# Kernel tuning notes

Hardware: AMD Instinct MI355X
Metric: run time of the kernel (lower is better)

Reference implementation:

```python
import jax, jax.numpy as jnp
import numpy as np
from jax import lax

L, C, H, W = 3, 64, 32, 32   # layer_num, new_size channels/spatial
N = H * W                    # 1024 attention positions
B = 8


def _conv(x, w, b, stride, pad):
    out = lax.conv_general_dilated(
        x, w, (stride, stride), [(pad, pad), (pad, pad)],
        dimension_numbers=('NCHW', 'OIHW', 'NCHW'))
    return out + b[None, :, None, None]


def setup_inputs() -> dict:
    key = jax.random.key(0)
    ks = iter(jax.random.split(key, 40))
    def rn(shape, scale=1.0):
        return (jax.random.normal(next(ks), shape) * scale).astype(jnp.float32)
    inp = {
        'src0': rn((B, 128, 64, 64)), 'src1': rn((B, 256, 32, 32)), 'src2': rn((B, 512, 32, 32)),
        'tgt0': rn((B, 128, 64, 64)), 'tgt1': rn((B, 256, 32, 32)), 'tgt2': rn((B, 512, 32, 32)),
    }
    # Project/Fit convs: layer0 is stride-2 3x3 (64->32), layers 1,2 are 1x1
    for pre, ic, k in [('fs0', 128, 3), ('fs1', 256, 1), ('fs2', 512, 1),
                       ('ft0', 128, 3), ('ft1', 256, 1), ('ft2', 512, 1)]:
        inp[pre + '_w'] = rn((C, ic, k, k), (ic * k * k) ** -0.5)
        inp[pre + '_b'] = rn((C,), 0.01)
    # PAM query/key/value and CAM value 1x1 convs, stacked over layers
    for pre in ['pq', 'pk', 'pv', 'cv']:
        inp[pre + '_w'] = rn((L, C, C), C ** -0.5)
        inp[pre + '_b'] = rn((L, C), 0.01)
    return inp


def reference(src0, src1, src2, tgt0, tgt1, tgt2,
              fs0_w, fs0_b, fs1_w, fs1_b, fs2_w, fs2_b,
              ft0_w, ft0_b, ft1_w, ft1_b, ft2_w, ft2_b,
              pq_w, pq_b, pk_w, pk_b, pv_w, pv_b, cv_w, cv_b):
    # Project: Fit each source/target to [B,C,H,W]
    S = jnp.stack([_conv(src0, fs0_w, fs0_b, 2, 1),
                   _conv(src1, fs1_w, fs1_b, 1, 0),
                   _conv(src2, fs2_w, fs2_b, 1, 0)])   # [L,B,C,H,W]
    T = jnp.stack([_conv(tgt0, ft0_w, ft0_b, 2, 1),
                   _conv(tgt1, ft1_w, ft1_b, 1, 0),
                   _conv(tgt2, ft2_w, ft2_b, 1, 0)])
    S = S.reshape(L, B, C, N)
    T = T.reshape(L, B, C, N)

    # ---- PAM: position attention over all (target i, source j) pairs ----
    q = jnp.einsum('ioc,ibcn->ibon', pq_w, T) + pq_b[:, None, :, None]
    k = jnp.einsum('joc,jbcn->jbon', pk_w, S) + pk_b[:, None, :, None]
    v = jnp.einsum('ioc,ibcn->ibon', pv_w, T) + pv_b[:, None, :, None]
    e_pam = jnp.einsum('ibcn,jbcm->ijbnm', q, k)          # [L,L,B,N,N]
    alpha_pam = jax.nn.softmax(lax.stop_gradient(e_pam.mean(axis=(2, 3, 4))), axis=-1)
    attn_pam = jax.nn.softmax(e_pam, axis=-1).sum(axis=1)  # sum over sources j -> [L,B,N,N]
    # out[b,c,n] = sum_m v[b,c,m] * attn[b,n,m]  (value @ attention^T)
    out_pam = jnp.einsum('ibcm,ibnm->ibcn', v, attn_pam)

    # ---- CAM: channel attention over all pairs ----
    e_cam = jnp.einsum('ibcn,jbdn->ijbcd', T, S)           # [L,L,B,C,C]
    alpha_cam = jax.nn.softmax(lax.stop_gradient(e_cam.mean(axis=(2, 3, 4))), axis=-1)
    attn_cam = jax.nn.softmax(e_cam, axis=-1).sum(axis=1)  # [L,B,C,C]
    vc = jnp.einsum('ioc,ibcn->ibon', cv_w, T) + cv_b[:, None, :, None]
    out_cam = jnp.einsum('ibcd,ibdn->ibcn', attn_cam, vc)

    fused = ((out_pam + out_cam) * 0.5).reshape(L, B, C * N)
    alpha = (alpha_cam + alpha_pam) * 0.5                  # [L,L]
    srcs = S.reshape(L, B, C * N)
    # DAAttention appends fused_i then projected target_i per layer (order preserved)
    tgts = jnp.stack([fused, T.reshape(L, B, C * N)], axis=1).reshape(2 * L, B, C * N)
    return (srcs, alpha, tgts)
```

## Files before the change

kernel.cpp:

```cpp
#include <hip/hip_runtime.h>

static constexpr int L_ = 3, B_ = 8, C_ = 64, N_ = 1024;
static constexpr int PLANE = C_ * N_;
static constexpr int SZ    = L_ * B_ * PLANE;
static constexpr int BPL   = B_ * PLANE;

#define DI __device__ __forceinline__

typedef _Float16 h8 __attribute__((ext_vector_type(8)));
typedef __attribute__((ext_vector_type(4))) float f32x4;
typedef unsigned int uint32;

DI float wred_sum(float v) {
#pragma unroll
  for (int m = 1; m < 64; m <<= 1) v += __shfl_xor(v, m, 64);
  return v;
}

DI unsigned short f2h(float f) {
  return __builtin_bit_cast(unsigned short, (_Float16)f);
}
DI uint32 pkh(float a, float b) {
  return (uint32)f2h(a) | ((uint32)f2h(b) << 16);
}
DI h8 bch8(uint4 v) { return __builtin_bit_cast(h8, v); }

DI f32x4 mfmah(h8 a, h8 b, f32x4 c) {
  return __builtin_amdgcn_mfma_f32_16x16x32_f16(a, b, c, 0, 0, 0);
}

__global__ __launch_bounds__(256) void xprep_kernel(
    const float* __restrict__ in, unsigned short* __restrict__ out, int K, int N)
{
  const int g = blockIdx.x, kc = blockIdx.y, nc = blockIdx.z;
  const int t = threadIdx.x;
  __shared__ float tl[64][65];
  const float* ing = in + (size_t)g * K * N + (size_t)(kc * 64) * N + nc * 64;
#pragma unroll 4
  for (int r = 0; r < 16; ++r) {
    const int kk = r * 4 + (t >> 6);
    tl[kk][t & 63] = ing[(size_t)kk * N + (t & 63)];
  }
  __syncthreads();
  const int mm = t >> 2, kseg = (t & 3) * 16;
  uint32 hw[8];
#pragma unroll
  for (int ii = 0; ii < 8; ++ii)
    hw[ii] = pkh(tl[kseg + 2 * ii][mm], tl[kseg + 2 * ii + 1][mm]);
  unsigned short* o = out + ((size_t)g * N + nc * 64 + mm) * K + kc * 64 + kseg;
  uint4 h0; h0.x = hw[0]; h0.y = hw[1]; h0.z = hw[2]; h0.w = hw[3];
  uint4 h1; h1.x = hw[4]; h1.y = hw[5]; h1.z = hw[6]; h1.w = hw[7];
  *reinterpret_cast<uint4*>(o)     = h0;
  *reinterpret_cast<uint4*>(o + 8) = h1;
}

__global__ __launch_bounds__(256) void w9conv_kernel(
    const float* __restrict__ w_s, const float* __restrict__ w_t,
    unsigned short* __restrict__ w9_s, unsigned short* __restrict__ w9_t)
{
  const int e = blockIdx.x * 256 + threadIdx.x;
  const float* w = (e < 73728) ? w_s : w_t;
  unsigned short* o = (e < 73728) ? w9_s : w9_t;
  const int le = (e < 73728) ? e : e - 73728;
  const int ci = le & 127;
  const int q = le >> 7;
  const int co = q & 63;
  const int k9 = q >> 6;
  o[le] = f2h(w[(co * 128 + ci) * 9 + k9]);
}

__global__ __launch_bounds__(256) void conv0_mfma_kernel(
    const unsigned short* __restrict__ inT_s, const unsigned short* __restrict__ inT_t,
    const unsigned short* __restrict__ w9_s, const unsigned short* __restrict__ w9_t,
    const float* __restrict__ b_s, const float* __restrict__ b_t,
    float* __restrict__ Sout, float* __restrict__ Tout, float* __restrict__ tdup)
{
  const int yr = blockIdx.x;
  const int b  = blockIdx.y;
  const int st = blockIdx.z;
  const unsigned short* inT = st ? inT_t : inT_s;
  const unsigned short* w9  = st ? w9_t  : w9_s;
  const float* bias = st ? b_t : b_s;
  float* outA = st ? Tout : Sout;

  const int t = threadIdx.x, lane = t & 63;
  const int ct = t >> 6;
  const int nl = lane & 15, g16 = lane >> 4;
  const unsigned short* inb = inT + (size_t)b * (4096 * 128);
  const unsigned short* wbase = w9 + (size_t)(ct * 16 + nl) * 128;

  f32x4 acc0 = f32x4{0.f, 0.f, 0.f, 0.f};
  f32x4 acc1 = f32x4{0.f, 0.f, 0.f, 0.f};
  const uint4 zz = uint4{0u, 0u, 0u, 0u};

#pragma unroll 1
  for (int tap = 0; tap < 9; ++tap) {
    const int ky = tap / 3, kx = tap - 3 * (tap / 3);
    const int py = 2 * yr - 1 + ky;
    const int px0 = 2 * nl - 1 + kx;
    const int px1 = px0 + 32;
    const bool v0 = (py >= 0) && (px0 >= 0);
    const bool v1 = (py >= 0);
    const unsigned short* prow = inb + (ptrdiff_t)py * (64 * 128);
#pragma unroll
    for (int ks = 0; ks < 4; ++ks) {
      const h8 a = bch8(*reinterpret_cast<const uint4*>(
          wbase + tap * 8192 + ks * 32 + g16 * 8));
      const uint4 bv0 = v0 ? *reinterpret_cast<const uint4*>(
                                 prow + px0 * 128 + ks * 32 + g16 * 8) : zz;
      const uint4 bv1 = v1 ? *reinterpret_cast<const uint4*>(
                                 prow + px1 * 128 + ks * 32 + g16 * 8) : zz;
      acc0 = mfmah(a, bch8(bv0), acc0);
      acc1 = mfmah(a, bch8(bv1), acc1);
    }
  }

  const int yb = yr * 32;
#pragma unroll
  for (int r = 0; r < 4; ++r) {
    const int co = ct * 16 + g16 * 4 + r;
    const float bv = bias[co];
    const int idx = (b * 64 + co) * 1024 + yb + nl;
    const float o0 = acc0[r] + bv;
    const float o1 = acc1[r] + bv;
    outA[idx] = o0; outA[idx + 16] = o1;
    if (st) { tdup[idx] = o0; tdup[idx + 16] = o1; }
  }
}

__global__ __launch_bounds__(256) void gemm64_kernel(
    const float* __restrict__ W, int wstride, int wdiv,
    const float* __restrict__ X, int xstride,
    float* __restrict__ out, int ostride,
    const float* __restrict__ bias, int bstride,
    int K)
{
  const int g  = blockIdx.x;
  const int n0 = blockIdx.y * 64;
  const float* Wg = W + (size_t)(g / wdiv) * wstride;
  const float* Xg = X + (size_t)g * xstride;
  const int t = threadIdx.x;
  __shared__ float Xs[32][64];
  __shared__ float Ws[32][64];
  const int tn = t & 15, cgp = t >> 4;
  const int n4 = tn * 4, co4 = cgp * 4;
  float acc[4][4] = {};

  for (int k0 = 0; k0 < K; k0 += 32) {
    {
      const int kk = t >> 4;
      const int nn = (t & 15) * 4;
      *reinterpret_cast<float4*>(&Xs[kk][nn]) =
          *reinterpret_cast<const float4*>(Xg + (size_t)(k0 + kk) * N_ + n0 + nn);
      *reinterpret_cast<float4*>(&Xs[kk + 16][nn]) =
          *reinterpret_cast<const float4*>(Xg + (size_t)(k0 + kk + 16) * N_ + n0 + nn);
    }
    {
      const int co = t & 63, q4 = t >> 6;
      const float* wp = Wg + (size_t)co * K + k0 + q4 * 8;
      const float4 a = *reinterpret_cast<const float4*>(wp);
      const float4 c = *reinterpret_cast<const float4*>(wp + 4);
      const int kb = q4 * 8;
      Ws[kb + 0][co] = a.x; Ws[kb + 1][co] = a.y; Ws[kb + 2][co] = a.z; Ws[kb + 3][co] = a.w;
      Ws[kb + 4][co] = c.x; Ws[kb + 5][co] = c.y; Ws[kb + 6][co] = c.z; Ws[kb + 7][co] = c.w;
    }
    __syncthreads();
#pragma unroll
    for (int kk = 0; kk < 32; ++kk) {
      const float4 xv = *reinterpret_cast<const float4*>(&Xs[kk][n4]);
      const float4 wv = *reinterpret_cast<const float4*>(&Ws[kk][co4]);
      const float xa[4] = {xv.x, xv.y, xv.z, xv.w};
      const float wa[4] = {wv.x, wv.y, wv.z, wv.w};
#pragma unroll
      for (int a = 0; a < 4; ++a)
#pragma unroll
        for (int b2 = 0; b2 < 4; ++b2)
          acc[a][b2] = fmaf(wa[a], xa[b2], acc[a][b2]);
    }
    __syncthreads();
  }

  float bv[4] = {0.f, 0.f, 0.f, 0.f};
  if (bias) {
    const float* bg = bias + (size_t)(g / wdiv) * bstride;
    bv[0] = bg[co4]; bv[1] = bg[co4 + 1]; bv[2] = bg[co4 + 2]; bv[3] = bg[co4 + 3];
  }
#pragma unroll
  for (int ii = 0; ii < 4; ++ii) {
    float4 o4;
    o4.x = acc[ii][0] + bv[ii]; o4.y = acc[ii][1] + bv[ii];
    o4.z = acc[ii][2] + bv[ii]; o4.w = acc[ii][3] + bv[ii];
    *reinterpret_cast<float4*>(out + (size_t)g * ostride + (co4 + ii) * N_ + n0 + n4) = o4;
  }
}

__global__ __launch_bounds__(256) void proj_kernel(
    const float* __restrict__ Tm, const float* __restrict__ Sm,
    const float* __restrict__ wq, const float* __restrict__ wk,
    const float* __restrict__ wv2, const float* __restrict__ wc,
    const float* __restrict__ bq, const float* __restrict__ bk,
    const float* __restrict__ bv2, const float* __restrict__ bc,
    float* __restrict__ outbase)
{
  const int g  = blockIdx.x;
  const int n0 = blockIdx.y * 64;
  const int z  = blockIdx.z;
  const float* W  = (z == 0) ? wq : (z == 1) ? wk : (z == 2) ? wv2 : wc;
  const float* bi = (z == 0) ? bq : (z == 1) ? bk : (z == 2) ? bv2 : bc;
  const float* Xg = ((z == 1) ? Sm : Tm) + (size_t)g * PLANE;
  float* out = outbase + (size_t)z * SZ + (size_t)g * PLANE;
  const float* Wg = W + (g >> 3) * 4096;
  const float* bg = bi + (g >> 3) * 64;

  const int t = threadIdx.x;
  __shared__ float Xs[32][64];
  __shared__ float Ws[32][64];
  const int tn = t & 15, cgp = t >> 4;
  const int n4 = tn * 4, co4 = cgp * 4;
  float acc[4][4] = {};

#pragma unroll 1
  for (int k0 = 0; k0 < 64; k0 += 32) {
    {
      const int kk = t >> 4;
      const int nn = (t & 15) * 4;
      *reinterpret_cast<float4*>(&Xs[kk][nn]) =
          *reinterpret_cast<const float4*>(Xg + (size_t)(k0 + kk) * N_ + n0 + nn);
      *reinterpret_cast<float4*>(&Xs[kk + 16][nn]) =
          *reinterpret_cast<const float4*>(Xg + (size_t)(k0 + kk + 16) * N_ + n0 + nn);
    }
    {
      const int co = t & 63, q4 = t >> 6;
      const float* wp = Wg + (size_t)co * 64 + k0 + q4 * 8;
      const float4 a = *reinterpret_cast<const float4*>(wp);
      const float4 c = *reinterpret_cast<const float4*>(wp + 4);
      const int kb = q4 * 8;
      Ws[kb + 0][co] = a.x; Ws[kb + 1][co] = a.y; Ws[kb + 2][co] = a.z; Ws[kb + 3][co] = a.w;
      Ws[kb + 4][co] = c.x; Ws[kb + 5][co] = c.y; Ws[kb + 6][co] = c.z; Ws[kb + 7][co] = c.w;
    }
    __syncthreads();
#pragma unroll
    for (int kk = 0; kk < 32; ++kk) {
      const float4 xv = *reinterpret_cast<const float4*>(&Xs[kk][n4]);
      const float4 wv = *reinterpret_cast<const float4*>(&Ws[kk][co4]);
      const float xa[4] = {xv.x, xv.y, xv.z, xv.w};
      const float wa[4] = {wv.x, wv.y, wv.z, wv.w};
#pragma unroll
      for (int a = 0; a < 4; ++a)
#pragma unroll
        for (int b2 = 0; b2 < 4; ++b2)
          acc[a][b2] = fmaf(wa[a], xa[b2], acc[a][b2]);
    }
    __syncthreads();
  }

#pragma unroll
  for (int ii = 0; ii < 4; ++ii) {
    const float bv = bg[co4 + ii];
    float4 o4;
    o4.x = acc[ii][0] + bv; o4.y = acc[ii][1] + bv;
    o4.z = acc[ii][2] + bv; o4.w = acc[ii][3] + bv;
    *reinterpret_cast<float4*>(out + (co4 + ii) * N_ + n0 + n4) = o4;
  }
}

__global__ __launch_bounds__(256) void whconv_kernel(
    const float* __restrict__ w1s, const float* __restrict__ w2s,
    const float* __restrict__ w1t, const float* __restrict__ w2t,
    unsigned short* __restrict__ wh)
{
  const int p = blockIdx.x * 256 + threadIdx.x;
  const float* in; int local; unsigned short* out;
  if (p < 8192)       { in = w1s; local = p;         out = wh; }
  else if (p < 24576) { in = w2s; local = p - 8192;  out = wh + 16384; }
  else if (p < 32768) { in = w1t; local = p - 24576; out = wh + 49152; }
  else                { in = w2t; local = p - 32768; out = wh + 65536; }
  const float2 v = *reinterpret_cast<const float2*>(in + 2 * local);
  *reinterpret_cast<uint32*>(out + 2 * local) = pkh(v.x, v.y);
}

__global__ __launch_bounds__(256) void gemmh_kernel(
    const unsigned short* __restrict__ Xa, const unsigned short* __restrict__ Xb,
    const unsigned short* __restrict__ Wa, const unsigned short* __restrict__ Wb,
    const float* __restrict__ ba, const float* __restrict__ bb,
    float* __restrict__ oa, float* __restrict__ ob, float* __restrict__ o2b,
    int K)
{
  const int g = blockIdx.x;
  const bool isb = g >= 8;
  const int gl = g & 7;
  const unsigned short* X = (isb ? Xb : Xa) + (size_t)gl * 1024 * K;
  const unsigned short* W = isb ? Wb : Wa;
  const float* bias = isb ? bb : ba;
  float* out = (isb ? ob : oa) + (size_t)gl * PLANE;
  float* out2 = isb ? o2b + (size_t)gl * PLANE : nullptr;

  const int t = threadIdx.x, lane = t & 63, wv = t >> 6;
  const int nl = lane & 15, g16 = lane >> 4;
  const int n0w = blockIdx.y * 64 + wv * 16;

  const unsigned short* xp = X + (size_t)(n0w + nl) * K + g16 * 8;
  const unsigned short* wp = W + (size_t)nl * K + g16 * 8;

  f32x4 acc[4];
#pragma unroll
  for (int ct = 0; ct < 4; ++ct) acc[ct] = f32x4{0.f, 0.f, 0.f, 0.f};

#pragma unroll 4
  for (int kk = 0; kk < K; kk += 32) {
    const h8 a = bch8(*reinterpret_cast<const uint4*>(xp + kk));
#pragma unroll
    for (int ct = 0; ct < 4; ++ct) {
      const h8 bfr = bch8(*reinterpret_cast<const uint4*>(wp + (size_t)ct * 16 * K + kk));
      acc[ct] = mfmah(a, bfr, acc[ct]);
    }
  }

#pragma unroll
  for (int ct = 0; ct < 4; ++ct) {
    const int co = ct * 16 + nl;
    const float bv = bias[co];
    float4 o4;
    o4.x = acc[ct][0] + bv; o4.y = acc[ct][1] + bv;
    o4.z = acc[ct][2] + bv; o4.w = acc[ct][3] + bv;
    const int idx = co * N_ + n0w + g16 * 4;
    *reinterpret_cast<float4*>(out + idx) = o4;
    if (out2) {
      out2[idx] = o4.x; out2[idx + 1] = o4.y;
      out2[idx + 2] = o4.z; out2[idx + 3] = o4.w;
    }
  }
}

__global__ __launch_bounds__(256) void kprep_kernel(
    const float* __restrict__ kb, const float* __restrict__ vb,
    unsigned short* __restrict__ kT, unsigned short* __restrict__ vh)
{
  const int g = blockIdx.x;
  const int ch = blockIdx.y;
  const int t = threadIdx.x;
  const float* kg = kb + (size_t)g * PLANE;
  __shared__ float tl[64][65];

#pragma unroll 1
  for (int tile = 0; tile < 4; ++tile) {
    const int m0 = ch * 256 + tile * 64;
    __syncthreads();
#pragma unroll 4
    for (int r = 0; r < 16; ++r) {
      const int c = r * 4 + (t >> 6);
      tl[c][t & 63] = kg[c * N_ + m0 + (t & 63)];
    }
    __syncthreads();
    const int mm = t >> 2, cseg = (t & 3) * 16;
    uint32 hw[8];
#pragma unroll
    for (int ii = 0; ii < 8; ++ii)
      hw[ii] = pkh(tl[cseg + 2 * ii][mm], tl[cseg + 2 * ii + 1][mm]);
    const size_t o = ((size_t)g * 1024 + m0 + mm) * 64 + cseg;
    uint4 h0; h0.x = hw[0]; h0.y = hw[1]; h0.z = hw[2]; h0.w = hw[3];
    uint4 h1; h1.x = hw[4]; h1.y = hw[5]; h1.z = hw[6]; h1.w = hw[7];
    *reinterpret_cast<uint4*>(kT + o)     = h0;
    *reinterpret_cast<uint4*>(kT + o + 8) = h1;
  }

  const float* vg = vb + (size_t)g * PLANE;
  unsigned short* vo = vh + (size_t)g * PLANE;
  for (int e8 = ch * 2048 + t; e8 < (ch + 1) * 2048; e8 += 256) {
    const float4 a = *reinterpret_cast<const float4*>(vg + (size_t)e8 * 8);
    const float4 b = *reinterpret_cast<const float4*>(vg + (size_t)e8 * 8 + 4);
    uint4 u;
    u.x = pkh(a.x, a.y); u.y = pkh(a.z, a.w);
    u.z = pkh(b.x, b.y); u.w = pkh(b.z, b.w);
    *reinterpret_cast<uint4*>(vo + (size_t)e8 * 8) = u;
  }
}

__global__ __launch_bounds__(256) void ecam_kernel(
    const float* __restrict__ T, const float* __restrict__ S,
    float* __restrict__ ecam, float* __restrict__ esum_cam)
{
  const int bx = blockIdx.x;
  const int b = bx & 7;
  const int j = (bx >> 3) % 3;
  const int i = bx / 24;
  const float* Tg = T + (size_t)(i * 8 + b) * PLANE;
  const float* Sg = S + (size_t)(j * 8 + b) * PLANE;
  const int t = threadIdx.x;
  __shared__ float Ts[64 * 68];
  __shared__ float Ss[64 * 68];
  __shared__ float rs[4];
  float acc[4][4] = {};
  const int c0 = (t & 15) * 4, d0 = (t >> 4) * 4;

  for (int nb = 0; nb < 1024; nb += 64) {
    __syncthreads();
    {
      const int nn = t & 63, rb = t >> 6;
#pragma unroll
      for (int r = 0; r < 16; ++r) {
        const int row = rb * 16 + r;
        Ts[nn * 68 + row] = Tg[row * N_ + nb + nn];
        Ss[nn * 68 + row] = Sg[row * N_ + nb + nn];
      }
    }
    __syncthreads();
#pragma unroll 8
    for (int nn = 0; nn < 64; ++nn) {
      const float4 tv = *reinterpret_cast<const float4*>(&Ts[nn * 68 + c0]);
      const float4 sv = *reinterpret_cast<const float4*>(&Ss[nn * 68 + d0]);
      const float ta[4] = {tv.x, tv.y, tv.z, tv.w};
      const float sa[4] = {sv.x, sv.y, sv.z, sv.w};
#pragma unroll
      for (int ci = 0; ci < 4; ++ci)
#pragma unroll
        for (int di = 0; di < 4; ++di)
          acc[ci][di] = fmaf(ta[ci], sa[di], acc[ci][di]);
    }
  }
  float s = 0.f;
#pragma unroll
  for (int ci = 0; ci < 4; ++ci)
#pragma unroll
    for (int di = 0; di < 4; ++di) s += acc[ci][di];
  s = wred_sum(s);
  if ((t & 63) == 0) rs[t >> 6] = s;
  __syncthreads();
  if (t == 0) atomicAdd(esum_cam + i * 3 + j, rs[0] + rs[1] + rs[2] + rs[3]);

  float* eo = ecam + (size_t)((i * 3 + j) * 8 + b) * 4096;
#pragma unroll
  for (int ci = 0; ci < 4; ++ci) {
    float4 o4; o4.x = acc[ci][0]; o4.y = acc[ci][1]; o4.z = acc[ci][2]; o4.w = acc[ci][3];
    *reinterpret_cast<float4*>(eo + (c0 + ci) * 64 + d0) = o4;
  }
}

__global__ __launch_bounds__(256) void acam_kernel(
    const float* __restrict__ ecam, float* __restrict__ acam)
{
  const int bx = blockIdx.x;
  const int b = bx & 7, i = bx >> 3;
  const int t = threadIdx.x;
  const int c = t >> 2, seg = t & 3;
  float acc[16] = {};
#pragma unroll
  for (int j = 0; j < 3; ++j) {
    const float* e = ecam + (size_t)((i * 3 + j) * 8 + b) * 4096 + c * 64 + seg * 16;
    float ev[16];
#pragma unroll
    for (int r = 0; r < 4; ++r) {
      const float4 v4 = *reinterpret_cast<const float4*>(e + r * 4);
      ev[4 * r] = v4.x; ev[4 * r + 1] = v4.y; ev[4 * r + 2] = v4.z; ev[4 * r + 3] = v4.w;
    }
    float mx = ev[0];
#pragma unroll
    for (int r = 1; r < 16; ++r) mx = fmaxf(mx, ev[r]);
    mx = fmaxf(mx, __shfl_xor(mx, 1, 4));
    mx = fmaxf(mx, __shfl_xor(mx, 2, 4));
    float pv[16], ss = 0.f;
#pragma unroll
    for (int r = 0; r < 16; ++r) { pv[r] = __expf(ev[r] - mx); ss += pv[r]; }
    ss += __shfl_xor(ss, 1, 4);
    ss += __shfl_xor(ss, 2, 4);
    const float rc = 1.f / ss;
#pragma unroll
    for (int r = 0; r < 16; ++r) acc[r] += pv[r] * rc;
  }
  float* ao = acam + (size_t)(i * 8 + b) * 4096 + c * 64 + seg * 16;
#pragma unroll
  for (int r = 0; r < 4; ++r) {
    float4 o4; o4.x = acc[4 * r]; o4.y = acc[4 * r + 1]; o4.z = acc[4 * r + 2]; o4.w = acc[4 * r + 3];
    *reinterpret_cast<float4*>(ao + r * 4) = o4;
  }
}

__global__ __launch_bounds__(512, 4) void pam_mfma_kernel(
    const float* __restrict__ q, const unsigned short* __restrict__ kT,
    const unsigned short* __restrict__ vh,
    const float* __restrict__ ocam, float* __restrict__ tgts, float* __restrict__ esum_pam)
{
  const int bx = blockIdx.x;
  const int qt = bx & 63;
  const int b  = (bx >> 6) & 7;
  const int i  = bx >> 9;
  const int n0 = qt * 16;
  const int t = threadIdx.x;
  const int lane = t & 63;
  const int wv = t >> 6;
  const int nl = lane & 15;
  const int g16 = lane >> 4;

  __shared__ unsigned short Plds[16 * 1024];
  __shared__ float qlds[64 * 17];
  __shared__ float redmx[128];
  __shared__ float redse[128];
  __shared__ float redes[8];
  float* osum = qlds;

  const size_t ibo = (size_t)(i * 8 + b) * PLANE;

  const float* qg = q + ibo;
  for (int e = t; e < 1024; e += 512)
    qlds[(e >> 4) * 17 + (e & 15)] = qg[(e >> 4) * N_ + n0 + (e & 15)];
  __syncthreads();

  h8 qh[2];
#pragma unroll
  for (int ks = 0; ks < 2; ++ks) {
#pragma unroll
    for (int idx = 0; idx < 8; ++idx)
      qh[ks][idx] = (_Float16)qlds[(ks * 32 + g16 * 8 + idx) * 17 + nl];
  }

  const int wm0 = wv * 128;
  const int ct = wv & 3;
  const int mh = wv >> 2;
  const unsigned short* vg = vh + ibo + (size_t)(ct * 16 + nl) * 1024 + mh * 512 + g16 * 8;
  f32x4 oat = f32x4{0.f, 0.f, 0.f, 0.f};

#pragma unroll 1
  for (int j = 0; j < 3; ++j) {
    const unsigned short* kp =
        kT + ((size_t)(j * 8 + b) * 1024 + wm0 + nl) * 64 + g16 * 8;

    f32x4 l4[8];
#pragma unroll
    for (int tt = 0; tt < 8; ++tt) {
      const int off = tt * 1024;
      const uint4 k0 = *reinterpret_cast<const uint4*>(kp + off);
      const uint4 k1 = *reinterpret_cast<const uint4*>(kp + off + 32);
      f32x4 a = f32x4{0.f, 0.f, 0.f, 0.f};
      a = mfmah(bch8(k0), qh[0], a);
      a = mfmah(bch8(k1), qh[1], a);
      l4[tt] = a;
    }

    float pm = -3.4e38f, es = 0.f;
#pragma unroll
    for (int tt = 0; tt < 8; ++tt) {
#pragma unroll
      for (int r = 0; r < 4; ++r) { pm = fmaxf(pm, l4[tt][r]); es += l4[tt][r]; }
    }
    pm = fmaxf(pm, __shfl_xor(pm, 16, 64));
    pm = fmaxf(pm, __shfl_xor(pm, 32, 64));
    es = wred_sum(es);
    if (lane < 16) redmx[wv * 16 + lane] = pm;
    if (lane == 0) redes[wv] = es;
    __syncthreads();
    float mx = redmx[nl];
#pragma unroll
    for (int w = 1; w < 8; ++w) mx = fmaxf(mx, redmx[w * 16 + nl]);
    if (t == 0) {
      float s = 0.f;
#pragma unroll
      for (int w = 0; w < 8; ++w) s += redes[w];
      atomicAdd(esum_pam + i * 3 + j, s);
    }

    float ps = 0.f;
#pragma unroll
    for (int tt = 0; tt < 8; ++tt) {
#pragma unroll
      for (int r = 0; r < 4; ++r) {
        l4[tt][r] = __expf(l4[tt][r] - mx);
        ps += l4[tt][r];
      }
    }
#pragma unroll
    for (int tt = 0; tt < 8; ++tt) {
      const int m = wm0 + tt * 16 + g16 * 4;
      uint2 w2;
      w2.x = pkh(l4[tt][0], l4[tt][1]);
      w2.y = pkh(l4[tt][2], l4[tt][3]);
      *reinterpret_cast<uint2*>(&Plds[nl * 1024 + (m ^ (nl * 8))]) = w2;
    }
    ps += __shfl_xor(ps, 16, 64);
    ps += __shfl_xor(ps, 32, 64);
    if (lane < 16) redse[wv * 16 + lane] = ps;
    __syncthreads();
    float den = redse[nl];
#pragma unroll
    for (int w = 1; w < 8; ++w) den += redse[w * 16 + nl];
    const float rs = 1.f / den;

    f32x4 oa = f32x4{0.f, 0.f, 0.f, 0.f};
    f32x4 ob = f32x4{0.f, 0.f, 0.f, 0.f};
#pragma unroll 4
    for (int ks = 0; ks < 16; ks += 2) {
      const int ml0 = mh * 512 + ks * 32 + g16 * 8;
      const int ml1 = ml0 + 32;
      const uint4 va0 = *reinterpret_cast<const uint4*>(vg + ks * 32);
      const uint4 pf0 = *reinterpret_cast<const uint4*>(&Plds[nl * 1024 + (ml0 ^ (nl * 8))]);
      const uint4 va1 = *reinterpret_cast<const uint4*>(vg + ks * 32 + 32);
      const uint4 pf1 = *reinterpret_cast<const uint4*>(&Plds[nl * 1024 + (ml1 ^ (nl * 8))]);
      oa = mfmah(bch8(va0), bch8(pf0), oa);
      ob = mfmah(bch8(va1), bch8(pf1), ob);
    }
#pragma unroll
    for (int r = 0; r < 4; ++r) oat[r] += rs * (oa[r] + ob[r]);
  }

  if (mh == 0) {
#pragma unroll
    for (int r = 0; r < 4; ++r)
      osum[(ct * 16 + g16 * 4 + r) * 16 + nl] = oat[r];
  }
  __syncthreads();
  if (mh == 1) {
    const float* og = ocam + ibo;
    float* outg = tgts + (size_t)(2 * i * 8 + b) * PLANE;
#pragma unroll
    for (int r = 0; r < 4; ++r) {
      const int c = ct * 16 + g16 * 4 + r;
      const int idx = c * N_ + n0 + nl;
      outg[idx] = 0.5f * (oat[r] + osum[c * 16 + nl] + og[idx]);
    }
  }
}

__global__ void alpha_kernel(const float* __restrict__ esum, float* __restrict__ alpha)
{
  const int t = threadIdx.x;
  if (t >= 9) return;
  const int i = t / 3, j = t % 3;
  float p[3], c[3];
#pragma unroll
  for (int jj = 0; jj < 3; ++jj) {
    p[jj] = esum[i * 3 + jj] * (1.0f / 8388608.0f);
    c[jj] = esum[9 + i * 3 + jj] * (1.0f / 32768.0f);
  }
  const float mp = fmaxf(p[0], fmaxf(p[1], p[2]));
  const float mc = fmaxf(c[0], fmaxf(c[1], c[2]));
  float sp = 0.f, sc = 0.f;
#pragma unroll
  for (int jj = 0; jj < 3; ++jj) { sp += __expf(p[jj] - mp); sc += __expf(c[jj] - mc); }
  alpha[t] = 0.5f * (__expf(p[j] - mp) / sp + __expf(c[j] - mc) / sc);
}

extern "C" void kernel_launch(void* const* d_in, const int* in_sizes, int n_in,
                              void* d_out, int out_size, void* d_ws, size_t ws_size,
                              hipStream_t stream)
{
  const float* src0 = (const float*)d_in[0];
  const float* src1 = (const float*)d_in[1];
  const float* src2 = (const float*)d_in[2];
  const float* tgt0 = (const float*)d_in[3];
  const float* tgt1 = (const float*)d_in[4];
  const float* tgt2 = (const float*)d_in[5];
  const float* fs0_w = (const float*)d_in[6];  const float* fs0_b = (const float*)d_in[7];
  const float* fs1_w = (const float*)d_in[8];  const float* fs1_b = (const float*)d_in[9];
  const float* fs2_w = (const float*)d_in[10]; const float* fs2_b = (const float*)d_in[11];
  const float* ft0_w = (const float*)d_in[12]; const float* ft0_b = (const float*)d_in[13];
  const float* ft1_w = (const float*)d_in[14]; const float* ft1_b = (const float*)d_in[15];
  const float* ft2_w = (const float*)d_in[16]; const float* ft2_b = (const float*)d_in[17];
  const float* pq_w = (const float*)d_in[18];  const float* pq_b = (const float*)d_in[19];
  const float* pk_w = (const float*)d_in[20];  const float* pk_b = (const float*)d_in[21];
  const float* pv_w = (const float*)d_in[22];  const float* pv_b = (const float*)d_in[23];
  const float* cv_w = (const float*)d_in[24];  const float* cv_b = (const float*)d_in[25];

  float* out = (float*)d_out;
  float* S     = out;
  float* alpha = out + SZ;
  float* tgts  = out + SZ + 9;

  float* ws   = (float*)d_ws;
  float* T    = ws;
  float* qb   = ws + (size_t)SZ;
  float* kb   = ws + (size_t)2 * SZ;
  float* vb   = ws + (size_t)3 * SZ;
  float* vcb  = ws + (size_t)4 * SZ;
  float* ocam = ws + (size_t)5 * SZ;
  float* ecam = ws + (size_t)6 * SZ;
  float* acam = ws + (size_t)6 * SZ + 294912;
  float* esum = ws + (size_t)6 * SZ + 393216;

  unsigned short* kT = (unsigned short*)(ws + (size_t)6 * SZ + 393216 + 256);
  unsigned short* vh = kT + (size_t)24 * PLANE;
  unsigned short* wh = vh + (size_t)24 * PLANE;
  unsigned short* w9s = wh + 98304;
  unsigned short* w9t = w9s + 73728;

  unsigned short* inTs = (unsigned short*)qb;
  unsigned short* inTt = inTs + 4194304;
  unsigned short* Xs1 = (unsigned short*)qb;
  unsigned short* Xs2 = Xs1 + 2097152;
  unsigned short* Xt1 = Xs1 + 6291456;
  unsigned short* Xt2 = Xs1 + 8388608;

  hipMemsetAsync(esum, 0, 18 * sizeof(float), stream);

  w9conv_kernel<<<576, 256, 0, stream>>>(fs0_w, ft0_w, w9s, w9t);
  xprep_kernel<<<dim3(8, 2, 64), 256, 0, stream>>>(src0, inTs, 128, 4096);
  xprep_kernel<<<dim3(8, 2, 64), 256, 0, stream>>>(tgt0, inTt, 128, 4096);
  conv0_mfma_kernel<<<dim3(32, 8, 2), 256, 0, stream>>>(
      inTs, inTt, w9s, w9t, fs0_b, ft0_b, S, T, tgts + (size_t)1 * BPL);

  xprep_kernel<<<dim3(8, 4, 16), 256, 0, stream>>>(src1, Xs1, 256, 1024);
  xprep_kernel<<<dim3(8, 8, 16), 256, 0, stream>>>(src2, Xs2, 512, 1024);
  xprep_kernel<<<dim3(8, 4, 16), 256, 0, stream>>>(tgt1, Xt1, 256, 1024);
  xprep_kernel<<<dim3(8, 8, 16), 256, 0, stream>>>(tgt2, Xt2, 512, 1024);
  whconv_kernel<<<192, 256, 0, stream>>>(fs1_w, fs2_w, ft1_w, ft2_w, wh);
  gemmh_kernel<<<dim3(16, 16), 256, 0, stream>>>(
      Xs1, Xt1, wh, wh + 49152, fs1_b, ft1_b,
      S + BPL, T + BPL, tgts + (size_t)3 * BPL, 256);
  gemmh_kernel<<<dim3(16, 16), 256, 0, stream>>>(
      Xs2, Xt2, wh + 16384, wh + 65536, fs2_b, ft2_b,
      S + 2 * BPL, T + 2 * BPL, tgts + (size_t)5 * BPL, 512);

  proj_kernel<<<dim3(24, 16, 4), 256, 0, stream>>>(
      T, S, pq_w, pk_w, pv_w, cv_w, pq_b, pk_b, pv_b, cv_b, qb);

  kprep_kernel<<<dim3(24, 4), 256, 0, stream>>>(kb, vb, kT, vh);

  ecam_kernel<<<72, 256, 0, stream>>>(T, S, ecam, esum + 9);
  acam_kernel<<<24, 256, 0, stream>>>(ecam, acam);
  gemm64_kernel<<<dim3(24, 16), 256, 0, stream>>>(acam, 4096, 1, vcb, PLANE, ocam, PLANE,
                                                  nullptr, 0, 64);

  pam_mfma_kernel<<<1536, 512, 0, stream>>>(qb, kT, vh, ocam, tgts, esum);

  alpha_kernel<<<1, 64, 0, stream>>>(esum, alpha);
}
```

Before: 364.5 us.

## Rewrite PAM attention as single-wave flash-style kernel with online softmax

The PAM attention kernel used 512-thread blocks where 8 waves split the key dimension and synchronized through LDS for max/sum reductions. It now runs one 64-lane wave per 16-query tile, streaming keys in chunks of 128 with an online (running-max) softmax and accumulating all 64 output channels in registers. This removes block-level barriers and the cross-wave output merge, and shrinks LDS to a small per-wave buffer. In exchange each wave does 8x more sequential work, the rescale cost is added, and there are far fewer waves in flight per CU to hide memory latency.

Result: slower. 416.1 us (+14.2%).

```diff
diff --git a/kernel.cpp b/kernel.cpp
--- a/kernel.cpp
+++ b/kernel.cpp
@@ -475,146 +475,132 @@
   }
 }
 
-__global__ __launch_bounds__(512, 4) void pam_mfma_kernel(
+__global__ __launch_bounds__(64, 2) void pam_flash_kernel(
     const float* __restrict__ q, const unsigned short* __restrict__ kT,
     const unsigned short* __restrict__ vh,
     const float* __restrict__ ocam, float* __restrict__ tgts, float* __restrict__ esum_pam)
 {
-  const int bx = blockIdx.x;
-  const int qt = bx & 63;
-  const int b  = (bx >> 6) & 7;
-  const int i  = bx >> 9;
+  const int tile = blockIdx.x;
+  const int qt = tile & 63;
+  const int b  = (tile >> 6) & 7;
+  const int i  = tile >> 9;
   const int n0 = qt * 16;
-  const int t = threadIdx.x;
-  const int lane = t & 63;
-  const int wv = t >> 6;
+  const int lane = threadIdx.x & 63;
   const int nl = lane & 15;
   const int g16 = lane >> 4;
 
-  __shared__ unsigned short Plds[16 * 1024];
-  __shared__ float qlds[64 * 17];
-  __shared__ float redmx[128];
-  __shared__ float redse[128];
-  __shared__ float redes[8];
-  float* osum = qlds;
+  __shared__ unsigned short Pw[16 * 128];
 
   const size_t ibo = (size_t)(i * 8 + b) * PLANE;
 
-  const float* qg = q + ibo;
-  for (int e = t; e < 1024; e += 512)
-    qlds[(e >> 4) * 17 + (e & 15)] = qg[(e >> 4) * N_ + n0 + (e & 15)];
-  __syncthreads();
-
+  const float* qg = q + ibo + n0 + nl;
   h8 qh[2];
 #pragma unroll
   for (int ks = 0; ks < 2; ++ks) {
 #pragma unroll
     for (int idx = 0; idx < 8; ++idx)
-      qh[ks][idx] = (_Float16)qlds[(ks * 32 + g16 * 8 + idx) * 17 + nl];
-  }
-
-  const int wm0 = wv * 128;
-  const int ct = wv & 3;
-  const int mh = wv >> 2;
-  const unsigned short* vg = vh + ibo + (size_t)(ct * 16 + nl) * 1024 + mh * 512 + g16 * 8;
-  f32x4 oat = f32x4{0.f, 0.f, 0.f, 0.f};
+      qh[ks][idx] = (_Float16)qg[(size_t)(ks * 32 + g16 * 8 + idx) * N_];
+  }
+
+  f32x4 oat[4];
+#pragma unroll
+  for (int ct = 0; ct < 4; ++ct) oat[ct] = f32x4{0.f, 0.f, 0.f, 0.f};
 
 #pragma unroll 1
   for (int j = 0; j < 3; ++j) {
-    const unsigned short* kp =
-        kT + ((size_t)(j * 8 + b) * 1024 + wm0 + nl) * 64 + g16 * 8;
-
-    f32x4 l4[8];
-#pragma unroll
-    for (int tt = 0; tt < 8; ++tt) {
-      const int off = tt * 1024;
-      const uint4 k0 = *reinterpret_cast<const uint4*>(kp + off);
-      const uint4 k1 = *reinterpret_cast<const uint4*>(kp + off + 32);
-      f32x4 a = f32x4{0.f, 0.f, 0.f, 0.f};
-      a = mfmah(bch8(k0), qh[0], a);
-      a = mfmah(bch8(k1), qh[1], a);
-      l4[tt] = a;
-    }
-
-    float pm = -3.4e38f, es = 0.f;
-#pragma unroll
-    for (int tt = 0; tt < 8; ++tt) {
-#pragma unroll
-      for (int r = 0; r < 4; ++r) { pm = fmaxf(pm, l4[tt][r]); es += l4[tt][r]; }
-    }
-    pm = fmaxf(pm, __shfl_xor(pm, 16, 64));
-    pm = fmaxf(pm, __shfl_xor(pm, 32, 64));
+    const unsigned short* kj = kT + ((size_t)(j * 8 + b) * 1024 + nl) * 64 + g16 * 8;
+    float runmx = -3.4e38f, den = 0.f, es = 0.f;
+    f32x4 oacc[4];
+#pragma unroll
+    for (int ct = 0; ct < 4; ++ct) oacc[ct] = f32x4{0.f, 0.f, 0.f, 0.f};
+
+#pragma unroll 1
+    for (int mc = 0; mc < 8; ++mc) {
+      const unsigned short* kp = kj + (size_t)(mc * 128) * 64;
+
+      f32x4 l4[8];
+#pragma unroll
+      for (int tt = 0; tt < 8; ++tt) {
+        const int off = tt * 1024;
+        const uint4 k0 = *reinterpret_cast<const uint4*>(kp + off);
+        const uint4 k1 = *reinterpret_cast<const uint4*>(kp + off + 32);
+        f32x4 a = f32x4{0.f, 0.f, 0.f, 0.f};
+        a = mfmah(bch8(k0), qh[0], a);
+        a = mfmah(bch8(k1), qh[1], a);
+        l4[tt] = a;
+      }
+
+      float cm = -3.4e38f, cs = 0.f;
+#pragma unroll
+      for (int tt = 0; tt < 8; ++tt) {
+#pragma unroll
+        for (int r = 0; r < 4; ++r) { cm = fmaxf(cm, l4[tt][r]); cs += l4[tt][r]; }
+      }
+      es += cs;
+      cm = fmaxf(cm, __shfl_xor(cm, 16, 64));
+      cm = fmaxf(cm, __shfl_xor(cm, 32, 64));
+      const float newmx = fmaxf(runmx, cm);
+      const float sc = __expf(runmx - newmx);
+
+      float psum = 0.f;
+#pragma unroll
+      for (int tt = 0; tt < 8; ++tt) {
+#pragma unroll
+        for (int r = 0; r < 4; ++r) {
+          l4[tt][r] = __expf(l4[tt][r] - newmx);
+          psum += l4[tt][r];
+        }
+      }
+      den = den * sc + psum;
+#pragma unroll
+      for (int ct = 0; ct < 4; ++ct)
+#pragma unroll
+        for (int r = 0; r < 4; ++r) oacc[ct][r] *= sc;
+
+#pragma unroll
+      for (int tt = 0; tt < 8; ++tt) {
+        const int ml = tt * 16 + g16 * 4;
+        uint2 w2;
+        w2.x = pkh(l4[tt][0], l4[tt][1]);
+        w2.y = pkh(l4[tt][2], l4[tt][3]);
+        *reinterpret_cast<uint2*>(&Pw[nl * 128 + (ml ^ (nl * 8))]) = w2;
+      }
+
+      const unsigned short* vgc = vh + ibo + (size_t)nl * 1024 + mc * 128 + g16 * 8;
+#pragma unroll 2
+      for (int ks = 0; ks < 4; ++ks) {
+        const h8 pf = bch8(*reinterpret_cast<const uint4*>(
+            &Pw[nl * 128 + ((ks * 32 + g16 * 8) ^ (nl * 8))]));
+#pragma unroll
+        for (int ct = 0; ct < 4; ++ct) {
+          const uint4 va = *reinterpret_cast<const uint4*>(vgc + (size_t)ct * 16384 + ks * 32);
+          oacc[ct] = mfmah(bch8(va), pf, oacc[ct]);
+        }
+      }
+      runmx = newmx;
+    }
+
+    den += __shfl_xor(den, 16, 64);
+    den += __shfl_xor(den, 32, 64);
+    const float rs = 1.f / den;
+#pragma unroll
+    for (int ct = 0; ct < 4; ++ct)
+#pragma unroll
+      for (int r = 0; r < 4; ++r) oat[ct][r] += rs * oacc[ct][r];
+
     es = wred_sum(es);
-    if (lane < 16) redmx[wv * 16 + lane] = pm;
-    if (lane == 0) redes[wv] = es;
-    __syncthreads();
-    float mx = redmx[nl];
-#pragma unroll
-    for (int w = 1; w < 8; ++w) mx = fmaxf(mx, redmx[w * 16 + nl]);
-    if (t == 0) {
-      float s = 0.f;
-#pragma unroll
-      for (int w = 0; w < 8; ++w) s += redes[w];
-      atomicAdd(esum_pam + i * 3 + j, s);
-    }
-
-    float ps = 0.f;
-#pragma unroll
-    for (int tt = 0; tt < 8; ++tt) {
-#pragma unroll
-      for (int r = 0; r < 4; ++r) {
-        l4[tt][r] = __expf(l4[tt][r] - mx);
-        ps += l4[tt][r];
-      }
-    }
-#pragma unroll
-    for (int tt = 0; tt < 8; ++tt) {
-      const int m = wm0 + tt * 16 + g16 * 4;
-      uint2 w2;
-      w2.x = pkh(l4[tt][0], l4[tt][1]);
-      w2.y = pkh(l4[tt][2], l4[tt][3]);
-      *reinterpret_cast<uint2*>(&Plds[nl * 1024 + (m ^ (nl * 8))]) = w2;
-    }
-    ps += __shfl_xor(ps, 16, 64);
-    ps += __shfl_xor(ps, 32, 64);
-    if (lane < 16) redse[wv * 16 + lane] = ps;
-    __syncthreads();
-    float den = redse[nl];
-#pragma unroll
-    for (int w = 1; w < 8; ++w) den += redse[w * 16 + nl];
-    const float rs = 1.f / den;
-
-    f32x4 oa = f32x4{0.f, 0.f, 0.f, 0.f};
-    f32x4 ob = f32x4{0.f, 0.f, 0.f, 0.f};
-#pragma unroll 4
-    for (int ks = 0; ks < 16; ks += 2) {
-      const int ml0 = mh * 512 + ks * 32 + g16 * 8;
-      const int ml1 = ml0 + 32;
-      const uint4 va0 = *reinterpret_cast<const uint4*>(vg + ks * 32);
-      const uint4 pf0 = *reinterpret_cast<const uint4*>(&Plds[nl * 1024 + (ml0 ^ (nl * 8))]);
-      const uint4 va1 = *reinterpret_cast<const uint4*>(vg + ks * 32 + 32);
-      const uint4 pf1 = *reinterpret_cast<const uint4*>(&Plds[nl * 1024 + (ml1 ^ (nl * 8))]);
-      oa = mfmah(bch8(va0), bch8(pf0), oa);
-      ob = mfmah(bch8(va1), bch8(pf1), ob);
-    }
-#pragma unroll
-    for (int r = 0; r < 4; ++r) oat[r] += rs * (oa[r] + ob[r]);
-  }
-
-  if (mh == 0) {
-#pragma unroll
-    for (int r = 0; r < 4; ++r)
-      osum[(ct * 16 + g16 * 4 + r) * 16 + nl] = oat[r];
-  }
-  __syncthreads();
-  if (mh == 1) {
-    const float* og = ocam + ibo;
-    float* outg = tgts + (size_t)(2 * i * 8 + b) * PLANE;
+    if (lane == 0) atomicAdd(esum_pam + i * 3 + j, es);
+  }
+
+  const float* og = ocam + ibo;
+  float* outg = tgts + (size_t)(2 * i * 8 + b) * PLANE;
+#pragma unroll
+  for (int ct = 0; ct < 4; ++ct) {
 #pragma unroll
     for (int r = 0; r < 4; ++r) {
       const int c = ct * 16 + g16 * 4 + r;
       const int idx = c * N_ + n0 + nl;
-      outg[idx] = 0.5f * (oat[r] + osum[c * 16 + nl] + og[idx]);
+      outg[idx] = 0.5f * (oat[ct][r] + og[idx]);
     }
   }
 }
@@ -718,7 +704,7 @@
   gemm64_kernel<<<dim3(24, 16), 256, 0, stream>>>(acam, 4096, 1, vcb, PLANE, ocam, PLANE,
                                                   nullptr, 0, 64);
 
-  pam_mfma_kernel<<<1536, 512, 0, stream>>>(qb, kT, vh, ocam, tgts, esum);
+  pam_flash_kernel<<<1536, 64, 0, stream>>>(qb, kT, vh, ocam, tgts, esum);
 
   alpha_kernel<<<1, 64, 0, stream>>>(esum, alpha);
 }
```

## Accumulate normalized softmax probabilities across sources before a single PV matmul

Applied to the files above, without the earlier changes.

Instead of running the value-times-attention MFMA pass once per source layer j, each source's softmax is normalized and summed into the fp16 probability tile in LDS, and a single PV matmul runs after the j loop. This cuts the PV MFMA work and the V global loads by a factor of three. K and V loads are also batched ahead of their MFMAs to raise memory-level parallelism. In exchange, each source's contribution is rounded to fp16 again on every read-modify-write of the summed probabilities, and each thread does an extra LDS read per accumulation.

Measured after the change: 327.8 us. -10.1%, faster.

```diff
diff --git a/kernel.cpp b/kernel.cpp
--- a/kernel.cpp
+++ b/kernel.cpp
@@ -19,6 +19,9 @@
 
 DI unsigned short f2h(float f) {
   return __builtin_bit_cast(unsigned short, (_Float16)f);
+}
+DI float h2f(unsigned short h) {
+  return (float)__builtin_bit_cast(_Float16, h);
 }
 DI uint32 pkh(float a, float b) {
   return (uint32)f2h(a) | ((uint32)f2h(b) << 16);
@@ -516,8 +519,6 @@
   const int wm0 = wv * 128;
   const int ct = wv & 3;
   const int mh = wv >> 2;
-  const unsigned short* vg = vh + ibo + (size_t)(ct * 16 + nl) * 1024 + mh * 512 + g16 * 8;
-  f32x4 oat = f32x4{0.f, 0.f, 0.f, 0.f};
 
 #pragma unroll 1
   for (int j = 0; j < 3; ++j) {
@@ -526,14 +527,21 @@
 
     f32x4 l4[8];
 #pragma unroll
-    for (int tt = 0; tt < 8; ++tt) {
-      const int off = tt * 1024;
-      const uint4 k0 = *reinterpret_cast<const uint4*>(kp + off);
-      const uint4 k1 = *reinterpret_cast<const uint4*>(kp + off + 32);
-      f32x4 a = f32x4{0.f, 0.f, 0.f, 0.f};
-      a = mfmah(bch8(k0), qh[0], a);
-      a = mfmah(bch8(k1), qh[1], a);
-      l4[tt] = a;
+    for (int hh = 0; hh < 2; ++hh) {
+      uint4 kf[8];
+#pragma unroll
+      for (int tt = 0; tt < 4; ++tt) {
+        const int off = (hh * 4 + tt) * 1024;
+        kf[2 * tt]     = *reinterpret_cast<const uint4*>(kp + off);
+        kf[2 * tt + 1] = *reinterpret_cast<const uint4*>(kp + off + 32);
+      }
+#pragma unroll
+      for (int tt = 0; tt < 4; ++tt) {
+        f32x4 a = f32x4{0.f, 0.f, 0.f, 0.f};
+        a = mfmah(bch8(kf[2 * tt]), qh[0], a);
+        a = mfmah(bch8(kf[2 * tt + 1]), qh[1], a);
+        l4[hh * 4 + tt] = a;
+      }
     }
 
     float pm = -3.4e38f, es = 0.f;
@@ -567,14 +575,6 @@
         ps += l4[tt][r];
       }
     }
-#pragma unroll
-    for (int tt = 0; tt < 8; ++tt) {
-      const int m = wm0 + tt * 16 + g16 * 4;
-      uint2 w2;
-      w2.x = pkh(l4[tt][0], l4[tt][1]);
-      w2.y = pkh(l4[tt][2], l4[tt][3]);
-      *reinterpret_cast<uint2*>(&Plds[nl * 1024 + (m ^ (nl * 8))]) = w2;
-    }
     ps += __shfl_xor(ps, 16, 64);
     ps += __shfl_xor(ps, 32, 64);
     if (lane < 16) redse[wv * 16 + lane] = ps;
@@ -584,27 +584,46 @@
     for (int w = 1; w < 8; ++w) den += redse[w * 16 + nl];
     const float rs = 1.f / den;
 
-    f32x4 oa = f32x4{0.f, 0.f, 0.f, 0.f};
-    f32x4 ob = f32x4{0.f, 0.f, 0.f, 0.f};
-#pragma unroll 4
-    for (int ks = 0; ks < 16; ks += 2) {
-      const int ml0 = mh * 512 + ks * 32 + g16 * 8;
-      const int ml1 = ml0 + 32;
-      const uint4 va0 = *reinterpret_cast<const uint4*>(vg + ks * 32);
-      const uint4 pf0 = *reinterpret_cast<const uint4*>(&Plds[nl * 1024 + (ml0 ^ (nl * 8))]);
-      const uint4 va1 = *reinterpret_cast<const uint4*>(vg + ks * 32 + 32);
-      const uint4 pf1 = *reinterpret_cast<const uint4*>(&Plds[nl * 1024 + (ml1 ^ (nl * 8))]);
-      oa = mfmah(bch8(va0), bch8(pf0), oa);
-      ob = mfmah(bch8(va1), bch8(pf1), ob);
-    }
-#pragma unroll
-    for (int r = 0; r < 4; ++r) oat[r] += rs * (oa[r] + ob[r]);
+#pragma unroll
+    for (int tt = 0; tt < 8; ++tt) {
+      const int m = wm0 + tt * 16 + g16 * 4;
+      unsigned short* pp = &Plds[nl * 1024 + (m ^ (nl * 8))];
+      float p0 = l4[tt][0] * rs, p1 = l4[tt][1] * rs;
+      float p2 = l4[tt][2] * rs, p3 = l4[tt][3] * rs;
+      if (j > 0) {
+        const uint2 old = *reinterpret_cast<const uint2*>(pp);
+        p0 += h2f((unsigned short)(old.x & 0xffffu));
+        p1 += h2f((unsigned short)(old.x >> 16));
+        p2 += h2f((unsigned short)(old.y & 0xffffu));
+        p3 += h2f((unsigned short)(old.y >> 16));
+      }
+      uint2 w2; w2.x = pkh(p0, p1); w2.y = pkh(p2, p3);
+      *reinterpret_cast<uint2*>(pp) = w2;
+    }
+  }
+
+  __syncthreads();
+
+  const unsigned short* vg = vh + ibo + (size_t)(ct * 16 + nl) * 1024 + mh * 512 + g16 * 8;
+  f32x4 oa = f32x4{0.f, 0.f, 0.f, 0.f};
+#pragma unroll
+  for (int hh = 0; hh < 2; ++hh) {
+    uint4 vf[8];
+#pragma unroll
+    for (int u = 0; u < 8; ++u)
+      vf[u] = *reinterpret_cast<const uint4*>(vg + (hh * 8 + u) * 32);
+#pragma unroll
+    for (int u = 0; u < 8; ++u) {
+      const int ml = mh * 512 + (hh * 8 + u) * 32 + g16 * 8;
+      const uint4 pf = *reinterpret_cast<const uint4*>(&Plds[nl * 1024 + (ml ^ (nl * 8))]);
+      oa = mfmah(bch8(vf[u]), bch8(pf), oa);
+    }
   }
 
   if (mh == 0) {
 #pragma unroll
     for (int r = 0; r < 4; ++r)
-      osum[(ct * 16 + g16 * 4 + r) * 16 + nl] = oat[r];
+      osum[(ct * 16 + g16 * 4 + r) * 16 + nl] = oa[r];
   }
   __syncthreads();
   if (mh == 1) {
@@ -614,7 +633,7 @@
     for (int r = 0; r < 4; ++r) {
       const int c = ct * 16 + g16 * 4 + r;
       const int idx = c * N_ + n0 + nl;
-      outg[idx] = 0.5f * (oat[r] + osum[c * 16 + nl] + og[idx]);
+      outg[idx] = 0.5f * (oa[r] + osum[c * 16 + nl] + og[idx]);
     }
   }
 }
```
